# Optimization experiments

Measured on AMD Instinct MI355X. Metric: run time of the kernel, lower is better.

The kernel has to match this reference:

```python
import jax, jax.numpy as jnp
import numpy as np

NUM_NODES = 100000
IN_DIM = 64
OUT_DIM = 64
NUM_EDGES = 1250000


def setup_inputs() -> dict:
    key = jax.random.key(0)
    k1, k2, k3, k4, k5 = jax.random.split(key, 5)
    x = jax.random.normal(k1, (NUM_NODES, IN_DIM), dtype=jnp.float32)
    edge_index = jax.random.randint(k2, (2, NUM_EDGES), 0, NUM_NODES, dtype=jnp.int32)
    # Linear params (PyTorch default init: uniform(-1/sqrt(in), 1/sqrt(in)))
    bound = 1.0 / np.sqrt(IN_DIM)
    W_self = jax.random.uniform(k3, (OUT_DIM, IN_DIM), minval=-bound, maxval=bound, dtype=jnp.float32)
    b_self = jax.random.uniform(k4, (OUT_DIM,), minval=-bound, maxval=bound, dtype=jnp.float32)
    W_neigh = jax.random.uniform(k5, (OUT_DIM, IN_DIM), minval=-bound, maxval=bound, dtype=jnp.float32)
    return {"x": x, "edge_index": edge_index, "W_self": W_self, "b_self": b_self, "W_neigh": W_neigh}


def reference(x, edge_index, W_self, b_self, W_neigh):
    # x: [N, D_in], edge_index: [2, E]
    src, dst = edge_index[0], edge_index[1]
    num_nodes = x.shape[0]
    x_src = x[src]  # [E, D_in] gather
    neigh_agg = jax.ops.segment_sum(x_src, dst, num_segments=num_nodes)  # [N, D_in]
    deg = jax.ops.segment_sum(jnp.ones_like(dst, dtype=x.dtype), dst, num_segments=num_nodes)
    deg = jnp.clip(deg, 1.0, None)[:, None]
    neigh_mean = neigh_agg / deg
    out = x @ W_self.T + b_self + neigh_mean @ W_neigh.T
    return jax.nn.relu(out)
```

## Files before the change

### kernel.cpp

```cpp
#include <hip/hip_runtime.h>


#define BKSH 10
#define BKN 1024
#define NBMAX 128
#define CAPE 14336
#define WPT (CAPE / 1024)
#define CHUNK 4096

typedef __attribute__((ext_vector_type(8))) short short8;
typedef __attribute__((ext_vector_type(4))) float floatx4;

static __device__ inline unsigned short f2bf(float f) {
  union { float f; unsigned int u; } v;
  v.f = f;
  unsigned int r = v.u + 0x7FFFu + ((v.u >> 16) & 1u);
  return (unsigned short)(r >> 16);
}

static __device__ inline short8 pack8(float4 a, float4 b) {
  short8 s;
  s[0] = (short)f2bf(a.x); s[1] = (short)f2bf(a.y);
  s[2] = (short)f2bf(a.z); s[3] = (short)f2bf(a.w);
  s[4] = (short)f2bf(b.x); s[5] = (short)f2bf(b.y);
  s[6] = (short)f2bf(b.z); s[7] = (short)f2bf(b.w);
  return s;
}

static __device__ inline void add8(float* a, short8 sv) {
  union { short8 s; unsigned int u[4]; } c; c.s = sv;
#pragma unroll
  for (int i = 0; i < 4; ++i) {
    a[2 * i]     += __uint_as_float(c.u[i] << 16);
    a[2 * i + 1] += __uint_as_float(c.u[i] & 0xFFFF0000u);
  }
}

__global__ __launch_bounds__(256) void x2bf_prep(const float* __restrict__ x,
                                                 unsigned short* __restrict__ xb,
                                                 long long n,
                                                 int* __restrict__ cursor,
                                                 const float* __restrict__ Wself,
                                                 const float* __restrict__ Wneigh,
                                                 unsigned short* __restrict__ wsb,
                                                 unsigned short* __restrict__ wnb) {
  int t = threadIdx.x;
  long long i = ((long long)blockIdx.x * 256 + t) * 8;
  if (i < n) {
    float4 a = *(const float4*)&x[i];
    float4 b = *(const float4*)&x[i + 4];
    *(short8*)&xb[i] = pack8(a, b);
  }
  if (blockIdx.x == gridDim.x - 1) {
    if (t < NBMAX) cursor[t] = t * CAPE;
    for (int g = t; g < 512; g += 256) {
      const float* p = &Wself[g * 8];
      *(short8*)&wsb[g * 8] = pack8(*(const float4*)p, *(const float4*)(p + 4));
      const float* q = &Wneigh[g * 8];
      *(short8*)&wnb[g * 8] = pack8(*(const float4*)q, *(const float4*)(q + 4));
    }
  }
}

__global__ __launch_bounds__(256) void bin_scatter(const int* __restrict__ src,
                                                   const int* __restrict__ dst,
                                                   int* __restrict__ cursor,
                                                   int* __restrict__ ebuf, int E, int NB) {
  __shared__ int h[NBMAX], loff[NBMAX], gbase[NBMAX];
  __shared__ int sbuf[CHUNK];
  int t = threadIdx.x;
  if (t < NBMAX) h[t] = 0;
  __syncthreads();

  int base = blockIdx.x * CHUNK;
  int myd[CHUNK / 256], mys[CHUNK / 256];
#pragma unroll
  for (int i = 0; i < CHUNK / 256; ++i) {
    int e = base + t + 256 * i;
    if (e < E) {
      myd[i] = dst[e];
      mys[i] = src[e];
      atomicAdd(&h[myd[i] >> BKSH], 1);
    } else myd[i] = -1;
  }
  __syncthreads();

  if (t < 64) {
    int i0 = 2 * t, i1 = 2 * t + 1;
    int v0 = h[i0], v1 = h[i1];
    int s = v0 + v1, inc = s;
#pragma unroll
    for (int off = 1; off < 64; off <<= 1) {
      int u = __shfl_up(inc, off, 64);
      if (t >= off) inc += u;
    }
    int ex = inc - s;
    loff[i0] = ex; loff[i1] = ex + v0;
  }
  __syncthreads();

  if (t < NB) {
    if (h[t] > 0) gbase[t] = atomicAdd(&cursor[t], h[t]);
  }
  if (t < NBMAX) h[t] = 0;
  __syncthreads();

#pragma unroll
  for (int i = 0; i < CHUNK / 256; ++i) {
    if (myd[i] >= 0) {
      int b = myd[i] >> BKSH;
      int p = atomicAdd(&h[b], 1);
      sbuf[loff[b] + p] = mys[i] | ((myd[i] & (BKN - 1)) << 17);
    }
  }
  __syncthreads();

  int w = t >> 6, lane = t & 63;
  for (int b = w; b < NB; b += 4) {
    int c = h[b], lo = loff[b], go = gbase[b];
    for (int j = lane; j < c; j += 64)
      ebuf[go + j] = sbuf[lo + j];
  }
}

__global__ __launch_bounds__(1024) void sb_csr(const int* __restrict__ cursor,
                                               const int* __restrict__ ebuf,
                                               int* __restrict__ col,
                                               int2* __restrict__ rowse, int N) {
  __shared__ int sbuf[CAPE];
  __shared__ int cnt[BKN];
  __shared__ int wsum[16];
  int b = blockIdx.x, t = threadIdx.x;
  int s = b * CAPE, e = cursor[b];
  int n = e - s;

  int my[WPT];
#pragma unroll
  for (int i = 0; i < WPT; ++i) {
    int j = s + t + (i << 10);
    my[i] = (j < e) ? ebuf[j] : -1;
  }

  cnt[t] = 0;
  __syncthreads();
#pragma unroll
  for (int i = 0; i < WPT; ++i)
    if (my[i] >= 0) atomicAdd(&cnt[(my[i] >> 17) & (BKN - 1)], 1);
  __syncthreads();

  int v = cnt[t];
  int lane = t & 63, w = t >> 6;
  int inc = v;
#pragma unroll
  for (int o = 1; o < 64; o <<= 1) {
    int u = __shfl_up(inc, o, 64);
    if (lane >= o) inc += u;
  }
  if (lane == 63) wsum[w] = inc;
  __syncthreads();
  if (t < 16) {
    int s0 = wsum[t], incw = s0;
#pragma unroll
    for (int o = 1; o < 16; o <<= 1) {
      int u = __shfl_up(incw, o, 64);
      if (t >= o) incw += u;
    }
    wsum[t] = incw - s0;
  }
  __syncthreads();
  int ex = wsum[w] + inc - v;
  int node = (b << BKSH) + t;
  if (node < N) rowse[node] = make_int2(s + ex, v);
  __syncthreads();
  cnt[t] = ex;
  __syncthreads();

#pragma unroll
  for (int i = 0; i < WPT; ++i) {
    if (my[i] >= 0) {
      int nl = (my[i] >> 17) & (BKN - 1);
      int p = atomicAdd(&cnt[nl], 1);
      sbuf[p] = my[i] & 0x1FFFF;
    }
  }
  __syncthreads();

  for (int j = t; j < n; j += 1024) col[s + j] = sbuf[j];
}

__global__ __launch_bounds__(256) void gcn_gather(const unsigned short* __restrict__ xb,
                                                  const int2* __restrict__ rowse,
                                                  const int* __restrict__ col,
                                                  unsigned short* __restrict__ aggb,
                                                  int N) {
  int gid = blockIdx.x * 256 + threadIdx.x;
  int node = gid >> 6;
  if (node >= N) return;
  int lane = threadIdx.x & 63;
  int o = lane >> 3, d = lane & 7;
  int2 se = rowse[node];
  int s = se.x, c = se.y, e = s + c;

  float a[8] = {0.f, 0.f, 0.f, 0.f, 0.f, 0.f, 0.f, 0.f};
  float b2[8] = {0.f, 0.f, 0.f, 0.f, 0.f, 0.f, 0.f, 0.f};
  int j = s + o;
  for (; j + 8 < e; j += 16) {
    int c0 = col[j], c1 = col[j + 8];
    short8 v0 = *(const short8*)&xb[(long long)c0 * 64 + d * 8];
    short8 v1 = *(const short8*)&xb[(long long)c1 * 64 + d * 8];
    add8(a, v0);
    add8(b2, v1);
  }
  for (; j < e; j += 8) {
    short8 v = *(const short8*)&xb[(long long)col[j] * 64 + d * 8];
    add8(a, v);
  }
#pragma unroll
  for (int k = 0; k < 8; ++k) a[k] += b2[k];

#pragma unroll
  for (int m = 8; m <= 32; m <<= 1) {
#pragma unroll
    for (int k = 0; k < 8; ++k) a[k] += __shfl_xor(a[k], m, 64);
  }

  if (o == 0) {
    float inv = 1.0f / fmaxf((float)c, 1.0f);
    short8 r;
#pragma unroll
    for (int k = 0; k < 8; ++k) r[k] = (short)f2bf(a[k] * inv);
    *(short8*)&aggb[(long long)node * 64 + d * 8] = r;
  }
}

__global__ __launch_bounds__(256) void gcn_gemm(const unsigned short* __restrict__ xb,
                                                const unsigned short* __restrict__ aggb,
                                                const unsigned short* __restrict__ wsb,
                                                const float* __restrict__ bself,
                                                const unsigned short* __restrict__ wnb,
                                                float* __restrict__ out, int N) {
  int lane = threadIdx.x & 63;
  int w = threadIdx.x >> 6;
  int tb = blockIdx.x * 64 + w * 16;
  int m = lane & 15, q = lane >> 4;

  long long rowA = (long long)min(tb + m, N - 1) * 64;
  short8 ax[2], aa[2];
#pragma unroll
  for (int ks = 0; ks < 2; ++ks) {
    ax[ks] = *(const short8*)&xb[rowA + ks * 32 + q * 8];
    aa[ks] = *(const short8*)&aggb[rowA + ks * 32 + q * 8];
  }

#pragma unroll
  for (int nt = 0; nt < 4; ++nt) {
    int ob = nt * 16;
    long long rowB = (long long)(ob + m) * 64;
    floatx4 acc = {0.f, 0.f, 0.f, 0.f};
#pragma unroll
    for (int ks = 0; ks < 2; ++ks) {
      short8 bw = *(const short8*)&wsb[rowB + ks * 32 + q * 8];
      acc = __builtin_amdgcn_mfma_f32_16x16x32_bf16(ax[ks], bw, acc, 0, 0, 0);
      short8 bn = *(const short8*)&wnb[rowB + ks * 32 + q * 8];
      acc = __builtin_amdgcn_mfma_f32_16x16x32_bf16(aa[ks], bn, acc, 0, 0, 0);
    }
    float bias = bself[ob + m];
#pragma unroll
    for (int r = 0; r < 4; ++r) {
      int node = tb + q * 4 + r;
      if (node < N) {
        float v = acc[r] + bias;
        out[(long long)node * 64 + ob + m] = fmaxf(v, 0.f);
      }
    }
  }
}

extern "C" void kernel_launch(void* const* d_in, const int* in_sizes, int n_in,
                              void* d_out, int out_size, void* d_ws, size_t ws_size,
                              hipStream_t stream) {
  const float* x      = (const float*)d_in[0];
  const int*   eidx   = (const int*)d_in[1];
  const float* Wself  = (const float*)d_in[2];
  const float* bself  = (const float*)d_in[3];
  const float* Wneigh = (const float*)d_in[4];
  float* out = (float*)d_out;

  const int N = in_sizes[0] / 64;
  const int E = in_sizes[1] / 2;
  const int* src = eidx;
  const int* dst = eidx + E;
  const int NB = (N + BKN - 1) / BKN;

  unsigned short* xb   = (unsigned short*)d_ws;
  unsigned short* aggb = xb + (size_t)N * 64;
  int* cursor   = (int*)(aggb + (size_t)N * 64);
  unsigned short* wsb = (unsigned short*)(cursor + NBMAX);
  unsigned short* wnb = wsb + 4096;
  int2* rowse   = (int2*)(wnb + 4096);
  int* ebuf     = (int*)(rowse + N);
  int* col      = ebuf + (size_t)NB * CAPE;

  long long nx = (long long)N * 64;
  int xblocks = (int)(nx / 8 + 255) / 256 + 1;
  x2bf_prep<<<xblocks, 256, 0, stream>>>(x, xb, nx, cursor, Wself, Wneigh, wsb, wnb);

  int cb = (E + CHUNK - 1) / CHUNK;
  bin_scatter<<<cb, 256, 0, stream>>>(src, dst, cursor, ebuf, E, NB);
  sb_csr<<<NB, 1024, 0, stream>>>(cursor, ebuf, col, rowse, N);
  gcn_gather<<<(int)((nx + 255) / 256), 256, 0, stream>>>(xb, rowse, col, aggb, N);
  gcn_gemm<<<(N + 63) / 64, 256, 0, stream>>>(xb, aggb, wsb, bself, wnb, out, N);
}
```

Baseline: 169.3 us.

## Fuse bf16 conversion with edge binning and shrink CSR buckets to 512 nodes

Merges the x/weight bf16 conversion kernel and the edge bin-scatter kernel into one launch, with separate block ranges doing each job, and moves the cursor initialisation to a memset so the scatter no longer depends on the conversion kernel. Buckets are halved to 512 nodes, which gives twice as many sb_csr blocks of 512 threads with smaller shared buffers, and scatter chunks are doubled to 8192 edges. The gather loop is also merged into a single predicated loop. The costs are a memset, more global cursor atomics, and the risk that the fixed CAPE capacity per bucket (7168) overflows on skewed graphs.

```diff
diff --git a/kernel.cpp b/kernel.cpp
--- a/kernel.cpp
+++ b/kernel.cpp
@@ -1,12 +1,13 @@
 #include <hip/hip_runtime.h>
 
 
-#define BKSH 10
-#define BKN 1024
-#define NBMAX 128
-#define CAPE 14336
-#define WPT (CAPE / 1024)
-#define CHUNK 4096
+#define BKSH 9
+#define BKN 512
+#define NBMAX 256
+#define CAPE 7168
+#define WPT (CAPE / BKN)
+#define CHUNK 8192
+#define EPT (CHUNK / 256)
 
 typedef __attribute__((ext_vector_type(8))) short short8;
 typedef __attribute__((ext_vector_type(4))) float floatx4;
@@ -36,46 +37,42 @@
   }
 }
 
-__global__ __launch_bounds__(256) void x2bf_prep(const float* __restrict__ x,
-                                                 unsigned short* __restrict__ xb,
-                                                 long long n,
-                                                 int* __restrict__ cursor,
-                                                 const float* __restrict__ Wself,
-                                                 const float* __restrict__ Wneigh,
-                                                 unsigned short* __restrict__ wsb,
-                                                 unsigned short* __restrict__ wnb) {
-  int t = threadIdx.x;
-  long long i = ((long long)blockIdx.x * 256 + t) * 8;
-  if (i < n) {
-    float4 a = *(const float4*)&x[i];
-    float4 b = *(const float4*)&x[i + 4];
-    *(short8*)&xb[i] = pack8(a, b);
-  }
-  if (blockIdx.x == gridDim.x - 1) {
-    if (t < NBMAX) cursor[t] = t * CAPE;
-    for (int g = t; g < 512; g += 256) {
-      const float* p = &Wself[g * 8];
-      *(short8*)&wsb[g * 8] = pack8(*(const float4*)p, *(const float4*)(p + 4));
-      const float* q = &Wneigh[g * 8];
-      *(short8*)&wnb[g * 8] = pack8(*(const float4*)q, *(const float4*)(q + 4));
-    }
-  }
-}
-
-__global__ __launch_bounds__(256) void bin_scatter(const int* __restrict__ src,
-                                                   const int* __restrict__ dst,
-                                                   int* __restrict__ cursor,
-                                                   int* __restrict__ ebuf, int E, int NB) {
+__global__ __launch_bounds__(256) void k1_prep(
+    const float* __restrict__ x, unsigned short* __restrict__ xb, long long n,
+    const float* __restrict__ Wself, const float* __restrict__ Wneigh,
+    unsigned short* __restrict__ wsb, unsigned short* __restrict__ wnb,
+    const int* __restrict__ src, const int* __restrict__ dst,
+    int* __restrict__ cursor, int* __restrict__ ebuf, int E, int NB, int SCB) {
   __shared__ int h[NBMAX], loff[NBMAX], gbase[NBMAX];
   __shared__ int sbuf[CHUNK];
   int t = threadIdx.x;
+  int bid = blockIdx.x;
+
+  if (bid >= SCB) {
+    long long i = ((long long)(bid - SCB) * 256 + t) * 8;
+    if (i < n) {
+      float4 a = *(const float4*)&x[i];
+      float4 b = *(const float4*)&x[i + 4];
+      *(short8*)&xb[i] = pack8(a, b);
+    }
+    if (bid == gridDim.x - 1) {
+      for (int g = t; g < 512; g += 256) {
+        const float* p = &Wself[g * 8];
+        *(short8*)&wsb[g * 8] = pack8(*(const float4*)p, *(const float4*)(p + 4));
+        const float* q = &Wneigh[g * 8];
+        *(short8*)&wnb[g * 8] = pack8(*(const float4*)q, *(const float4*)(q + 4));
+      }
+    }
+    return;
+  }
+
   if (t < NBMAX) h[t] = 0;
   __syncthreads();
 
-  int base = blockIdx.x * CHUNK;
-  int myd[CHUNK / 256], mys[CHUNK / 256];
-#pragma unroll
-  for (int i = 0; i < CHUNK / 256; ++i) {
+  int base = bid * CHUNK;
+  int myd[EPT], mys[EPT];
+#pragma unroll
+  for (int i = 0; i < EPT; ++i) {
     int e = base + t + 256 * i;
     if (e < E) {
       myd[i] = dst[e];
@@ -86,27 +83,28 @@
   __syncthreads();
 
   if (t < 64) {
-    int i0 = 2 * t, i1 = 2 * t + 1;
-    int v0 = h[i0], v1 = h[i1];
-    int s = v0 + v1, inc = s;
+    int i0 = 4 * t;
+    int v0 = h[i0], v1 = h[i0 + 1], v2 = h[i0 + 2], v3 = h[i0 + 3];
+    int s4 = v0 + v1 + v2 + v3, inc = s4;
 #pragma unroll
     for (int off = 1; off < 64; off <<= 1) {
       int u = __shfl_up(inc, off, 64);
       if (t >= off) inc += u;
     }
-    int ex = inc - s;
-    loff[i0] = ex; loff[i1] = ex + v0;
+    int ex = inc - s4;
+    loff[i0] = ex; loff[i0 + 1] = ex + v0;
+    loff[i0 + 2] = ex + v0 + v1; loff[i0 + 3] = ex + v0 + v1 + v2;
   }
   __syncthreads();
 
   if (t < NB) {
-    if (h[t] > 0) gbase[t] = atomicAdd(&cursor[t], h[t]);
+    if (h[t] > 0) gbase[t] = t * CAPE + atomicAdd(&cursor[t], h[t]);
   }
   if (t < NBMAX) h[t] = 0;
   __syncthreads();
 
 #pragma unroll
-  for (int i = 0; i < CHUNK / 256; ++i) {
+  for (int i = 0; i < EPT; ++i) {
     if (myd[i] >= 0) {
       int b = myd[i] >> BKSH;
       int p = atomicAdd(&h[b], 1);
@@ -123,21 +121,22 @@
   }
 }
 
-__global__ __launch_bounds__(1024) void sb_csr(const int* __restrict__ cursor,
-                                               const int* __restrict__ ebuf,
-                                               int* __restrict__ col,
-                                               int2* __restrict__ rowse, int N) {
+__global__ __launch_bounds__(512) void sb_csr(const int* __restrict__ cursor,
+                                              const int* __restrict__ ebuf,
+                                              int* __restrict__ col,
+                                              int2* __restrict__ rowse, int N) {
   __shared__ int sbuf[CAPE];
   __shared__ int cnt[BKN];
-  __shared__ int wsum[16];
+  __shared__ int wsum[8];
   int b = blockIdx.x, t = threadIdx.x;
-  int s = b * CAPE, e = cursor[b];
-  int n = e - s;
+  int s = b * CAPE;
+  int n = cursor[b];
+  int e = s + n;
 
   int my[WPT];
 #pragma unroll
   for (int i = 0; i < WPT; ++i) {
-    int j = s + t + (i << 10);
+    int j = s + t + i * BKN;
     my[i] = (j < e) ? ebuf[j] : -1;
   }
 
@@ -158,10 +157,10 @@
   }
   if (lane == 63) wsum[w] = inc;
   __syncthreads();
-  if (t < 16) {
+  if (t < 8) {
     int s0 = wsum[t], incw = s0;
 #pragma unroll
-    for (int o = 1; o < 16; o <<= 1) {
+    for (int o = 1; o < 8; o <<= 1) {
       int u = __shfl_up(incw, o, 64);
       if (t >= o) incw += u;
     }
@@ -185,7 +184,7 @@
   }
   __syncthreads();
 
-  for (int j = t; j < n; j += 1024) col[s + j] = sbuf[j];
+  for (int j = t; j < n; j += BKN) col[s + j] = sbuf[j];
 }
 
 __global__ __launch_bounds__(256) void gcn_gather(const unsigned short* __restrict__ xb,
@@ -203,17 +202,14 @@
 
   float a[8] = {0.f, 0.f, 0.f, 0.f, 0.f, 0.f, 0.f, 0.f};
   float b2[8] = {0.f, 0.f, 0.f, 0.f, 0.f, 0.f, 0.f, 0.f};
-  int j = s + o;
-  for (; j + 8 < e; j += 16) {
-    int c0 = col[j], c1 = col[j + 8];
+  for (int j = s + o; j < e; j += 16) {
+    int c0 = col[j];
+    bool h2 = (j + 8) < e;
+    int c1 = h2 ? col[j + 8] : c0;
     short8 v0 = *(const short8*)&xb[(long long)c0 * 64 + d * 8];
     short8 v1 = *(const short8*)&xb[(long long)c1 * 64 + d * 8];
     add8(a, v0);
-    add8(b2, v1);
-  }
-  for (; j < e; j += 8) {
-    short8 v = *(const short8*)&xb[(long long)col[j] * 64 + d * 8];
-    add8(a, v);
+    if (h2) add8(b2, v1);
   }
 #pragma unroll
   for (int k = 0; k < 8; ++k) a[k] += b2[k];
@@ -301,13 +297,14 @@
   int* ebuf     = (int*)(rowse + N);
   int* col      = ebuf + (size_t)NB * CAPE;
 
+  hipMemsetAsync(cursor, 0, NBMAX * sizeof(int), stream);
+
   long long nx = (long long)N * 64;
-  int xblocks = (int)(nx / 8 + 255) / 256 + 1;
-  x2bf_prep<<<xblocks, 256, 0, stream>>>(x, xb, nx, cursor, Wself, Wneigh, wsb, wnb);
-
-  int cb = (E + CHUNK - 1) / CHUNK;
-  bin_scatter<<<cb, 256, 0, stream>>>(src, dst, cursor, ebuf, E, NB);
-  sb_csr<<<NB, 1024, 0, stream>>>(cursor, ebuf, col, rowse, N);
+  const int SCB = (E + CHUNK - 1) / CHUNK;
+  int xbl = (int)((nx / 8 + 255) / 256);
+  k1_prep<<<SCB + xbl + 1, 256, 0, stream>>>(x, xb, nx, Wself, Wneigh, wsb, wnb,
+                                             src, dst, cursor, ebuf, E, NB, SCB);
+  sb_csr<<<NB, BKN, 0, stream>>>(cursor, ebuf, col, rowse, N);
   gcn_gather<<<(int)((nx + 255) / 256), 256, 0, stream>>>(xb, rowse, col, aggb, N);
   gcn_gemm<<<(N + 63) / 64, 256, 0, stream>>>(xb, aggb, wsb, bself, wnb, out, N);
 }
```

Result: no change. 168.9 us (-0.3%).
